# Kernel optimization log

Measured on AMD Instinct MI355X. Metric: run time of the kernel, lower is better.

The kernel has to match this reference:

```python
import jax, jax.numpy as jnp
import numpy as np

EPS = 1e-5
DG = 2  # deformable_groups (num_group)


def conv3x3(x, w):
    return jax.lax.conv_general_dilated(x, w, (1, 1), ((1, 1), (1, 1)),
                                        dimension_numbers=('NCHW', 'OIHW', 'NCHW'))


def bn(x, g, b):
    # training-mode batch norm (batch statistics)
    m = x.mean(axis=(0, 2, 3), keepdims=True)
    v = x.var(axis=(0, 2, 3), keepdims=True)
    return g[None, :, None, None] * (x - m) / jnp.sqrt(v + EPS) + b[None, :, None, None]


def mod_deform_conv(x, w_off, b_off, w, b, dg):
    # ModulatedDeformConvPack: 3x3, stride 1, pad 1
    B, C, H, W = x.shape
    K = 9
    Cg = C // dg
    om = conv3x3(x, w_off) + b_off[None, :, None, None]        # [B, 3*dg*K, H, W]
    o1, o2, m = jnp.split(om, 3, axis=1)
    offy = o1.reshape(B, dg, K, H, W)
    offx = o2.reshape(B, dg, K, H, W)
    mask = jax.nn.sigmoid(m).reshape(B, dg, K, H, W)
    ky = (jnp.arange(K) // 3 - 1).astype(x.dtype)
    kx = (jnp.arange(K) % 3 - 1).astype(x.dtype)
    hh = jnp.arange(H, dtype=x.dtype)
    ww = jnp.arange(W, dtype=x.dtype)
    # fractional sample positions per tap: [B, dg, K, H, W]
    py = hh[None, None, None, :, None] + ky[None, None, :, None, None] + offy
    px = ww[None, None, None, None, :] + kx[None, None, :, None, None] + offx
    y0 = jnp.floor(py)
    x0 = jnp.floor(px)
    ly = py - y0
    lx = px - x0
    y0i = y0.astype(jnp.int32)
    x0i = x0.astype(jnp.int32)
    xg = x.reshape(B, dg, Cg, H * W)

    def gather(yi, xi):
        valid = ((yi >= 0) & (yi < H) & (xi >= 0) & (xi < W)).astype(x.dtype)
        idx = jnp.clip(yi, 0, H - 1) * W + jnp.clip(xi, 0, W - 1)
        flat = idx.reshape(B, dg, 1, K * H * W)
        v = jnp.take_along_axis(xg, flat, axis=3).reshape(B, dg, Cg, K, H, W)
        return v * valid[:, :, None]

    w00 = ((1 - ly) * (1 - lx))[:, :, None]
    w01 = ((1 - ly) * lx)[:, :, None]
    w10 = (ly * (1 - lx))[:, :, None]
    w11 = (ly * lx)[:, :, None]
    val = (gather(y0i, x0i) * w00 + gather(y0i, x0i + 1) * w01 +
           gather(y0i + 1, x0i) * w10 + gather(y0i + 1, x0i + 1) * w11)
    val = val * mask[:, :, None]                               # [B, dg, Cg, K, H, W]
    O = w.shape[0]
    out = jnp.einsum('ogck,bgckhw->bohw', w.reshape(O, dg, Cg, K), val)
    return out + b[None, :, None, None]


def setup_inputs() -> dict:
    key = jax.random.key(0)
    ks = jax.random.split(key, 24)
    B, inC, H, W = 64, 3, 64, 64
    K = 9
    d = {}
    d['x'] = jax.random.normal(ks[0], (B, inC, H, W), dtype=jnp.float32)
    d['conv1_w'] = jax.random.normal(ks[1], (8, inC, 3, 3), jnp.float32) * 0.1
    d['bn1_g'] = jnp.ones((8,), jnp.float32)
    d['bn1_b'] = jnp.zeros((8,), jnp.float32)
    d['conv2_w'] = jax.random.normal(ks[2], (20, 8, 3, 3), jnp.float32) * 0.1
    d['conv2_b'] = jnp.zeros((20,), jnp.float32)
    d['bn2_g'] = jnp.ones((20,), jnp.float32)
    d['bn2_b'] = jnp.zeros((20,), jnp.float32)
    d['off1_w'] = jax.random.normal(ks[3], (3 * DG * K, 20, 3, 3), jnp.float32) * 0.01
    d['off1_b'] = jnp.zeros((3 * DG * K,), jnp.float32)
    d['d1_w'] = jax.random.normal(ks[4], (40, 20, 3, 3), jnp.float32) * 0.05
    d['d1_b'] = jnp.zeros((40,), jnp.float32)
    d['bn3_g'] = jnp.ones((40,), jnp.float32)
    d['bn3_b'] = jnp.zeros((40,), jnp.float32)
    d['off2_w'] = jax.random.normal(ks[5], (3 * DG * K, 40, 3, 3), jnp.float32) * 0.01
    d['off2_b'] = jnp.zeros((3 * DG * K,), jnp.float32)
    d['d2_w'] = jax.random.normal(ks[6], (64, 40, 3, 3), jnp.float32) * 0.05
    d['d2_b'] = jnp.zeros((64,), jnp.float32)
    d['bn4_g'] = jnp.ones((64,), jnp.float32)
    d['bn4_b'] = jnp.zeros((64,), jnp.float32)
    d['fc_w'] = jax.random.normal(ks[7], (10, 256), jnp.float32) * 0.05
    d['fc_b'] = jnp.zeros((10,), jnp.float32)
    return d


def reference(x, conv1_w, bn1_g, bn1_b, conv2_w, conv2_b, bn2_g, bn2_b,
              off1_w, off1_b, d1_w, d1_b, bn3_g, bn3_b,
              off2_w, off2_b, d2_w, d2_b, bn4_g, bn4_b, fc_w, fc_b):
    h = bn(jax.nn.relu(conv3x3(x, conv1_w)), bn1_g, bn1_b)
    h = bn(jax.nn.relu(conv3x3(h, conv2_w) + conv2_b[None, :, None, None]), bn2_g, bn2_b)
    h = bn(jax.nn.relu(mod_deform_conv(h, off1_w, off1_b, d1_w, d1_b, DG)), bn3_g, bn3_b)
    h = bn(jax.nn.relu(mod_deform_conv(h, off2_w, off2_b, d2_w, d2_b, DG)), bn4_g, bn4_b)
    em = h
    B, C, H, W = h.shape
    # avg_pool2d with kernel [H//2, W//2] -> 2x2 spatial output
    p = h.reshape(B, C, 2, H // 2, 2, W // 2).mean(axis=(3, 5)).reshape(B, C * 4)
    logits = p @ fc_w.T + fc_b
    return jax.nn.softmax(logits, axis=1), em
```

## Files before the change

### kernel.cpp

```cpp
#include <hip/hip_runtime.h>
#include <math.h>

#define B_  64
#define H_  64
#define W_  64
#define HW  4096
#define NPIX 262144.0f

__global__ __launch_bounds__(256) void wtr_k(
    const float* __restrict__ w, float* __restrict__ wT, int O, int CK)
{
    const int i = blockIdx.x * 256 + threadIdx.x;
    if (i < O * CK) {
        const int o = i / CK, ck = i - o * CK;
        wT[ck * O + o] = w[i];
    }
}

template<int CT>
__device__ __forceinline__ void stats_accum(
    const float* res, float* sacc, float* ls, int tid)
{
    if (tid < 2 * CT) ls[tid] = 0.f;
    __syncthreads();
#pragma unroll
    for (int o = 0; o < CT; ++o) {
        float s = res[o], s2 = res[o] * res[o];
        for (int off = 32; off; off >>= 1) {
            s  += __shfl_down(s,  off);
            s2 += __shfl_down(s2, off);
        }
        if ((tid & 63) == 0) {
            atomicAdd(&ls[2 * o],     s);
            atomicAdd(&ls[2 * o + 1], s2);
        }
    }
    __syncthreads();
    if (tid < 2 * CT) atomicAdd(&sacc[tid], ls[tid]);
}

template<int C>
__global__ __launch_bounds__(64) void bn_fin_k(
    const float* __restrict__ sacc, float* __restrict__ st)
{
    const int t = threadIdx.x;
    if (t < C) {
        const float mean = sacc[2 * t] / NPIX;
        const float var  = sacc[2 * t + 1] / NPIX - mean * mean;
        st[t]     = mean;
        st[C + t] = rsqrtf(var + 1e-5f);
    }
}

__global__ __launch_bounds__(256) void conv1_k(
    const float* __restrict__ x, const float* __restrict__ w,
    float* __restrict__ out, float* __restrict__ sacc)
{
    const int tid = threadIdx.x;
    const int pix = blockIdx.x * 256 + tid;
    const int b   = blockIdx.y;
    const int h   = pix >> 6, ww = pix & 63;

    float acc[8];
#pragma unroll
    for (int o = 0; o < 8; ++o) acc[o] = 0.f;

#pragma unroll
    for (int ci = 0; ci < 3; ++ci) {
        const float* xp = x + ((size_t)b * 3 + ci) * HW;
#pragma unroll
        for (int t = 0; t < 9; ++t) {
            const int yy = h + t / 3 - 1, xx = ww + t % 3 - 1;
            const bool ok = (yy >= 0) && (yy < 64) && (xx >= 0) && (xx < 64);
            const float xv = ok ? xp[min(max(yy,0),63) * 64 + min(max(xx,0),63)] : 0.f;
#pragma unroll
            for (int o = 0; o < 8; ++o)
                acc[o] = fmaf(w[o * 27 + ci * 9 + t], xv, acc[o]);
        }
    }

    float res[8];
    float* ob = out + (size_t)b * 8 * HW + pix;
#pragma unroll
    for (int o = 0; o < 8; ++o) {
        res[o] = fmaxf(acc[o], 0.f);
        ob[(size_t)o * HW] = res[o];
    }

    __shared__ float ls[16];
    stats_accum<8>(res, sacc, ls, tid);
}

template<int CIN, int COUT, bool RELU, bool STATS>
__global__ __launch_bounds__(256, 4) void convn_k(
    const float* __restrict__ x, const float* __restrict__ wT,
    const float* __restrict__ bias, const float* __restrict__ st,
    const float* __restrict__ gg, const float* __restrict__ bb,
    float* __restrict__ out, float* __restrict__ sacc)
{
    const int tid = threadIdx.x;
    const int pix = blockIdx.x * 256 + tid;
    const int b   = blockIdx.y;
    const int h   = pix >> 6, ww = pix & 63;

    int  tpix[9];
    bool tok[9];
#pragma unroll
    for (int t = 0; t < 9; ++t) {
        const int yy = h + t / 3 - 1, xx = ww + t % 3 - 1;
        tok[t]  = (yy >= 0) && (yy < 64) && (xx >= 0) && (xx < 64);
        tpix[t] = min(max(yy, 0), 63) * 64 + min(max(xx, 0), 63);
    }

    float acc[COUT];
#pragma unroll
    for (int o = 0; o < COUT; ++o) acc[o] = bias[o];

    const float* xb = x + (size_t)b * CIN * HW;

    for (int ci = 0; ci < CIN; ++ci) {
        const float mean = st[ci], rstd = st[CIN + ci];
        const float a  = gg[ci] * rstd;
        const float cc = bb[ci] - gg[ci] * mean * rstd;
        const float* xp = xb + (size_t)ci * HW;

        float xv[9];
#pragma unroll
        for (int t = 0; t < 9; ++t)
            xv[t] = tok[t] ? fmaf(a, xp[tpix[t]], cc) : 0.f;

#pragma unroll
        for (int t = 0; t < 9; ++t) {
            const float* wp = wT + (ci * 9 + t) * COUT;
#pragma unroll
            for (int o = 0; o < COUT; ++o)
                acc[o] = fmaf(wp[o], xv[t], acc[o]);
        }
    }

    float res[COUT];
    float* ob = out + (size_t)b * COUT * HW + pix;
#pragma unroll
    for (int o = 0; o < COUT; ++o) {
        res[o] = RELU ? fmaxf(acc[o], 0.f) : acc[o];
        ob[(size_t)o * HW] = res[o];
    }

    if (STATS) {
        __shared__ float ls[2 * COUT];
        stats_accum<COUT>(res, sacc, ls, tid);
    }
}

template<int CG, int O, int VL, bool STATS>
__global__ __launch_bounds__(256, 4) void deform_k(
    const float* __restrict__ x, const float* __restrict__ om,
    const float* __restrict__ wT, const float* __restrict__ bias,
    const float* __restrict__ st, const float* __restrict__ gg,
    const float* __restrict__ bb,
    float* __restrict__ out, float* __restrict__ sacc)
{
    constexpr int CIN = 2 * CG;
    const int tid = threadIdx.x;
    const int pix = blockIdx.x * 256 + tid;
    const int b   = blockIdx.y;
    const int h   = pix >> 6, ww = pix & 63;

    float acc[O];
#pragma unroll
    for (int o = 0; o < O; ++o) acc[o] = bias[o];

    const float* omb = om + (size_t)b * 54 * HW + pix;
    const float* xb  = x + (size_t)b * CIN * HW;

    for (int g = 0; g < 2; ++g) {
#pragma unroll
        for (int k = 0; k < 9; ++k) {
            const int gk = g * 9 + k;
            const float offy = omb[(size_t)gk * HW];
            const float offx = omb[(size_t)(18 + gk) * HW];
            const float mraw = omb[(size_t)(36 + gk) * HW];
            const float msk  = 1.f / (1.f + __expf(-mraw));

            const float py = (float)(h + k / 3 - 1) + offy;
            const float px = (float)(ww + k % 3 - 1) + offx;
            const float y0f = floorf(py), x0f = floorf(px);
            const float ly = py - y0f, lx = px - x0f;
            const int y0 = (int)y0f, x0 = (int)x0f;
            const int y1 = y0 + 1,  x1 = x0 + 1;

            const bool y0ok = (y0 >= 0) && (y0 < 64);
            const bool y1ok = (y1 >= 0) && (y1 < 64);
            const bool x0ok = (x0 >= 0) && (x0 < 64);
            const bool x1ok = (x1 >= 0) && (x1 < 64);

            float w00 = (1.f-ly)*(1.f-lx)*msk; if (!(y0ok&&x0ok)) w00 = 0.f;
            float w01 = (1.f-ly)*lx      *msk; if (!(y0ok&&x1ok)) w01 = 0.f;
            float w10 = ly*(1.f-lx)      *msk; if (!(y1ok&&x0ok)) w10 = 0.f;
            float w11 = ly*lx            *msk; if (!(y1ok&&x1ok)) w11 = 0.f;
            const float wsum = w00 + w01 + w10 + w11;

            const int i00 = min(max(y0,0),63) * 64 + min(max(x0,0),63);
            const int dx  = (min(max(x1,0),63) - min(max(x0,0),63));
            const int dy  = (min(max(y1,0),63) - min(max(y0,0),63)) * 64;

            for (int cb = 0; cb < CG / VL; ++cb) {
                const int c0 = g * CG + cb * VL;

                float v00[VL], v01[VL], v10[VL], v11[VL];
#pragma unroll
                for (int j = 0; j < VL; ++j) {
                    const float* xp = xb + (size_t)(c0 + j) * HW + i00;
                    v00[j] = xp[0];
                    v01[j] = xp[dx];
                    v10[j] = xp[dy];
                    v11[j] = xp[dy + dx];
                }

                float val[VL];
#pragma unroll
                for (int j = 0; j < VL; ++j) {
                    const float mean = st[c0 + j], rstd = st[CIN + c0 + j];
                    const float a  = gg[c0 + j] * rstd;
                    const float cc = bb[c0 + j] - gg[c0 + j] * mean * rstd;
                    const float gath = w00*v00[j] + w01*v01[j] +
                                       w10*v10[j] + w11*v11[j];
                    val[j] = fmaf(a, gath, cc * wsum);
                }

                const float* wp0 = wT + ((c0 + 0) * 9 + k) * O;
                const float* wp1 = wT + ((c0 + 1) * 9 + k) * O;
#pragma unroll
                for (int o = 0; o < O; ++o) {
                    float t = acc[o];
                    t = fmaf(wp0[o], val[0], t);
                    t = fmaf(wp1[o], val[1], t);
                    if (VL == 4) {
                        t = fmaf(wp1[O * 9 + o], val[2], t);
                        t = fmaf(wp1[2 * O * 9 + o], val[3], t);
                    }
                    acc[o] = t;
                }
            }
        }
    }

    float res[O];
    float* ob = out + (size_t)b * O * HW + pix;
#pragma unroll
    for (int o = 0; o < O; ++o) {
        res[o] = fmaxf(acc[o], 0.f);
        ob[(size_t)o * HW] = res[o];
    }

    if (STATS) {
        __shared__ float ls[2 * O];
        stats_accum<O>(res, sacc, ls, tid);
    }
}

__global__ __launch_bounds__(256) void bn_apply4_k(
    float* __restrict__ y, const float* __restrict__ st,
    const float* __restrict__ gg, const float* __restrict__ bb)
{
    const size_t i4 = (size_t)blockIdx.x * 256 + threadIdx.x;
    const int c = (int)((i4 >> 10) & 63);
    const float m = st[c], r = st[64 + c];
    const float a = gg[c] * r, cc = bb[c] - gg[c] * m * r;
    float4 v = ((float4*)y)[i4];
    v.x = a*v.x + cc; v.y = a*v.y + cc; v.z = a*v.z + cc; v.w = a*v.w + cc;
    ((float4*)y)[i4] = v;
}

__global__ __launch_bounds__(256) void pool_k(
    const float* __restrict__ em, float* __restrict__ pooled)
{
    const int b = blockIdx.x, c = blockIdx.y, t = threadIdx.x;
    const int q = t >> 6, l = t & 63;
    const float* p = em + ((size_t)b * 64 + c) * HW + (q >> 1) * 32 * W_ + (q & 1) * 32;
    float s = 0.f;
    for (int i = l; i < 1024; i += 64) {
        const int yy = i >> 5, xx = i & 31;
        s += p[yy * W_ + xx];
    }
    for (int off = 32; off; off >>= 1) s += __shfl_down(s, off);
    if (l == 0) pooled[b * 256 + c * 4 + q] = s * (1.f / 1024.f);
}

__global__ __launch_bounds__(64) void fc_k(
    const float* __restrict__ pooled, const float* __restrict__ fcw,
    const float* __restrict__ fcb, float* __restrict__ out)
{
    const int b = blockIdx.x, t = threadIdx.x;
    __shared__ float logits[10];
    if (t < 10) {
        float l = fcb[t];
        const float* p = pooled + b * 256;
        for (int j = 0; j < 256; ++j) l += fcw[t * 256 + j] * p[j];
        logits[t] = l;
    }
    __syncthreads();
    if (t == 0) {
        float mx = logits[0];
        for (int i = 1; i < 10; ++i) mx = fmaxf(mx, logits[i]);
        float e[10]; float sum = 0.f;
        for (int i = 0; i < 10; ++i) { e[i] = __expf(logits[i] - mx); sum += e[i]; }
        const float inv = 1.f / sum;
        for (int i = 0; i < 10; ++i) out[b * 10 + i] = e[i] * inv;
    }
}

extern "C" void kernel_launch(void* const* d_in, const int* in_sizes, int n_in,
                              void* d_out, int out_size, void* d_ws, size_t ws_size,
                              hipStream_t stream)
{
    const float* x       = (const float*)d_in[0];
    const float* conv1_w = (const float*)d_in[1];
    const float* bn1_g   = (const float*)d_in[2];
    const float* bn1_b   = (const float*)d_in[3];
    const float* conv2_w = (const float*)d_in[4];
    const float* conv2_b = (const float*)d_in[5];
    const float* bn2_g   = (const float*)d_in[6];
    const float* bn2_b   = (const float*)d_in[7];
    const float* off1_w  = (const float*)d_in[8];
    const float* off1_b  = (const float*)d_in[9];
    const float* d1_w    = (const float*)d_in[10];
    const float* d1_b    = (const float*)d_in[11];
    const float* bn3_g   = (const float*)d_in[12];
    const float* bn3_b   = (const float*)d_in[13];
    const float* off2_w  = (const float*)d_in[14];
    const float* off2_b  = (const float*)d_in[15];
    const float* d2_w    = (const float*)d_in[16];
    const float* d2_b    = (const float*)d_in[17];
    const float* bn4_g   = (const float*)d_in[18];
    const float* bn4_b   = (const float*)d_in[19];
    const float* fc_w    = (const float*)d_in[20];
    const float* fc_b    = (const float*)d_in[21];

    float* ws = (float*)d_ws;
    float* Bb = ws;
    float* D  = ws + 5242880;
    float* C  = ws + 15728640;
    float* A  = C;
    float* sm = ws + 29884416;
    float* s1 = sm,        *s2 = sm + 16,  *s3 = sm + 56,  *s4 = sm + 136;
    float* st1 = sm + 264, *st2 = sm + 280, *st3 = sm + 320, *st4 = sm + 400;
    float* pooled = sm + 528;
    float* c2T = sm + 16912;
    float* o1T = sm + 18352;
    float* o2T = sm + 28072;
    float* d1T = sm + 47512;
    float* d2T = sm + 54712;

    float* outp = (float*)d_out;
    float* em   = outp + 640;

    const dim3 blk(256);
    const dim3 gpix(16, B_);

    hipMemsetAsync(sm, 0, 264 * sizeof(float), stream);

    wtr_k<<<(20*72  + 255)/256, blk, 0, stream>>>(conv2_w, c2T, 20, 72);
    wtr_k<<<(54*180 + 255)/256, blk, 0, stream>>>(off1_w,  o1T, 54, 180);
    wtr_k<<<(54*360 + 255)/256, blk, 0, stream>>>(off2_w,  o2T, 54, 360);
    wtr_k<<<(40*180 + 255)/256, blk, 0, stream>>>(d1_w,    d1T, 40, 180);
    wtr_k<<<(64*360 + 255)/256, blk, 0, stream>>>(d2_w,    d2T, 64, 360);

    conv1_k<<<gpix, blk, 0, stream>>>(x, conv1_w, A, s1);
    bn_fin_k<8><<<1, 64, 0, stream>>>(s1, st1);

    convn_k<8, 20, true, true><<<gpix, blk, 0, stream>>>(
        A, c2T, conv2_b, st1, bn1_g, bn1_b, Bb, s2);
    bn_fin_k<20><<<1, 64, 0, stream>>>(s2, st2);

    convn_k<20, 54, false, false><<<gpix, blk, 0, stream>>>(
        Bb, o1T, off1_b, st2, bn2_g, bn2_b, C, nullptr);
    deform_k<10, 40, 2, true><<<gpix, blk, 0, stream>>>(
        Bb, C, d1T, d1_b, st2, bn2_g, bn2_b, D, s3);
    bn_fin_k<40><<<1, 64, 0, stream>>>(s3, st3);

    convn_k<40, 54, false, false><<<gpix, blk, 0, stream>>>(
        D, o2T, off2_b, st3, bn3_g, bn3_b, C, nullptr);
    deform_k<20, 64, 4, true><<<gpix, blk, 0, stream>>>(
        D, C, d2T, d2_b, st3, bn3_g, bn3_b, em, s4);
    bn_fin_k<64><<<1, 64, 0, stream>>>(s4, st4);

    bn_apply4_k<<<16384, blk, 0, stream>>>(em, st4, bn4_g, bn4_b);

    pool_k<<<dim3(B_, 64), blk, 0, stream>>>(em, pooled);
    fc_k<<<B_, 64, 0, stream>>>(pooled, fc_w, fc_b, outp);
}
```

Before: 889.8 us.

## Use packed fp16 dot2 with channel-paired weights in conv and deform kernels

Weights are repacked into fp16 pairs of adjacent input channels, and activations are converted to packed half2 so each FMA pair becomes one v_dot2 instruction accumulating in fp32. BN scale/shift per channel is precomputed into shared memory once per block instead of being recomputed inside the loops, and the convn loop order is swapped to tap-outer. This halves the inner-loop ALU instruction count and weight load bandwidth, but reduces input and weight precision to fp16, which could raise numerical error. Full unrolling also increases code size and register pressure.

```diff
diff --git a/kernel.cpp b/kernel.cpp
--- a/kernel.cpp
+++ b/kernel.cpp
@@ -7,13 +7,23 @@
 #define HW  4096
 #define NPIX 262144.0f
 
-__global__ __launch_bounds__(256) void wtr_k(
-    const float* __restrict__ w, float* __restrict__ wT, int O, int CK)
+typedef __fp16 h2 __attribute__((ext_vector_type(2)));
+
+__global__ __launch_bounds__(256) void wpack_k(
+    const float* __restrict__ w, h2* __restrict__ wp, int O, int C)
 {
     const int i = blockIdx.x * 256 + threadIdx.x;
-    if (i < O * CK) {
-        const int o = i / CK, ck = i - o * CK;
-        wT[ck * O + o] = w[i];
+    const int total = 9 * (C / 2) * O;
+    if (i < total) {
+        const int o    = i % O;
+        const int rest = i / O;
+        const int cp   = rest % (C / 2);
+        const int t    = rest / (C / 2);
+        const int c    = 2 * cp;
+        h2 p;
+        p.x = (__fp16)w[o * (C * 9) + c * 9 + t];
+        p.y = (__fp16)w[o * (C * 9) + (c + 1) * 9 + t];
+        wp[i] = p;
     }
 }
 
@@ -93,7 +103,7 @@
 
 template<int CIN, int COUT, bool RELU, bool STATS>
 __global__ __launch_bounds__(256, 4) void convn_k(
-    const float* __restrict__ x, const float* __restrict__ wT,
+    const float* __restrict__ x, const h2* __restrict__ wp,
     const float* __restrict__ bias, const float* __restrict__ st,
     const float* __restrict__ gg, const float* __restrict__ bb,
     float* __restrict__ out, float* __restrict__ sacc)
@@ -103,6 +113,14 @@
     const int b   = blockIdx.y;
     const int h   = pix >> 6, ww = pix & 63;
 
+    __shared__ float lsa[CIN], lsc[CIN];
+    if (tid < CIN) {
+        const float mean = st[tid], rstd = st[CIN + tid];
+        lsa[tid] = gg[tid] * rstd;
+        lsc[tid] = bb[tid] - gg[tid] * mean * rstd;
+    }
+    __syncthreads();
+
     int  tpix[9];
     bool tok[9];
 #pragma unroll
@@ -118,23 +136,22 @@
 
     const float* xb = x + (size_t)b * CIN * HW;
 
-    for (int ci = 0; ci < CIN; ++ci) {
-        const float mean = st[ci], rstd = st[CIN + ci];
-        const float a  = gg[ci] * rstd;
-        const float cc = bb[ci] - gg[ci] * mean * rstd;
-        const float* xp = xb + (size_t)ci * HW;
-
-        float xv[9];
-#pragma unroll
-        for (int t = 0; t < 9; ++t)
-            xv[t] = tok[t] ? fmaf(a, xp[tpix[t]], cc) : 0.f;
-
-#pragma unroll
-        for (int t = 0; t < 9; ++t) {
-            const float* wp = wT + (ci * 9 + t) * COUT;
+#pragma unroll
+    for (int t = 0; t < 9; ++t) {
+        const float* xq = xb + tpix[t];
+        const bool ok = tok[t];
+#pragma unroll
+        for (int cp = 0; cp < CIN / 2; ++cp) {
+            const int c = 2 * cp;
+            const float x0 = xq[(size_t)c * HW];
+            const float x1 = xq[(size_t)(c + 1) * HW];
+            const float v0 = ok ? fmaf(lsa[c],     x0, lsc[c])     : 0.f;
+            const float v1 = ok ? fmaf(lsa[c + 1], x1, lsc[c + 1]) : 0.f;
+            const h2 val2 = __builtin_amdgcn_cvt_pkrtz(v0, v1);
+            const h2* wrow = wp + (t * (CIN / 2) + cp) * COUT;
 #pragma unroll
             for (int o = 0; o < COUT; ++o)
-                acc[o] = fmaf(wp[o], xv[t], acc[o]);
+                acc[o] = __builtin_amdgcn_fdot2(val2, wrow[o], acc[o], false);
         }
     }
 
@@ -152,10 +169,10 @@
     }
 }
 
-template<int CG, int O, int VL, bool STATS>
+template<int CG, int O, bool STATS>
 __global__ __launch_bounds__(256, 4) void deform_k(
     const float* __restrict__ x, const float* __restrict__ om,
-    const float* __restrict__ wT, const float* __restrict__ bias,
+    const h2* __restrict__ wp, const float* __restrict__ bias,
     const float* __restrict__ st, const float* __restrict__ gg,
     const float* __restrict__ bb,
     float* __restrict__ out, float* __restrict__ sacc)
@@ -165,6 +182,14 @@
     const int pix = blockIdx.x * 256 + tid;
     const int b   = blockIdx.y;
     const int h   = pix >> 6, ww = pix & 63;
+
+    __shared__ float lsa[CIN], lsc[CIN];
+    if (tid < CIN) {
+        const float mean = st[tid], rstd = st[CIN + tid];
+        lsa[tid] = gg[tid] * rstd;
+        lsc[tid] = bb[tid] - gg[tid] * mean * rstd;
+    }
+    __syncthreads();
 
     float acc[O];
 #pragma unroll
@@ -204,43 +229,27 @@
             const int dx  = (min(max(x1,0),63) - min(max(x0,0),63));
             const int dy  = (min(max(y1,0),63) - min(max(y0,0),63)) * 64;
 
-            for (int cb = 0; cb < CG / VL; ++cb) {
-                const int c0 = g * CG + cb * VL;
-
-                float v00[VL], v01[VL], v10[VL], v11[VL];
-#pragma unroll
-                for (int j = 0; j < VL; ++j) {
-                    const float* xp = xb + (size_t)(c0 + j) * HW + i00;
-                    v00[j] = xp[0];
-                    v01[j] = xp[dx];
-                    v10[j] = xp[dy];
-                    v11[j] = xp[dy + dx];
-                }
-
-                float val[VL];
-#pragma unroll
-                for (int j = 0; j < VL; ++j) {
-                    const float mean = st[c0 + j], rstd = st[CIN + c0 + j];
-                    const float a  = gg[c0 + j] * rstd;
-                    const float cc = bb[c0 + j] - gg[c0 + j] * mean * rstd;
-                    const float gath = w00*v00[j] + w01*v01[j] +
-                                       w10*v10[j] + w11*v11[j];
-                    val[j] = fmaf(a, gath, cc * wsum);
-                }
-
-                const float* wp0 = wT + ((c0 + 0) * 9 + k) * O;
-                const float* wp1 = wT + ((c0 + 1) * 9 + k) * O;
-#pragma unroll
-                for (int o = 0; o < O; ++o) {
-                    float t = acc[o];
-                    t = fmaf(wp0[o], val[0], t);
-                    t = fmaf(wp1[o], val[1], t);
-                    if (VL == 4) {
-                        t = fmaf(wp1[O * 9 + o], val[2], t);
-                        t = fmaf(wp1[2 * O * 9 + o], val[3], t);
-                    }
-                    acc[o] = t;
-                }
+#pragma unroll
+            for (int cp = 0; cp < CG / 2; ++cp) {
+                const int c = g * CG + 2 * cp;
+                const float* xp0 = xb + (size_t)c * HW + i00;
+                const float* xp1 = xp0 + HW;
+
+                const float a00 = xp0[0],  a01 = xp0[dx];
+                const float a10 = xp0[dy], a11 = xp0[dy + dx];
+                const float b00 = xp1[0],  b01 = xp1[dx];
+                const float b10 = xp1[dy], b11 = xp1[dy + dx];
+
+                const float g0 = w00*a00 + w01*a01 + w10*a10 + w11*a11;
+                const float g1 = w00*b00 + w01*b01 + w10*b10 + w11*b11;
+                const float v0 = fmaf(lsa[c],     g0, lsc[c]     * wsum);
+                const float v1 = fmaf(lsa[c + 1], g1, lsc[c + 1] * wsum);
+                const h2 val2 = __builtin_amdgcn_cvt_pkrtz(v0, v1);
+
+                const h2* wrow = wp + (k * (CIN / 2) + (c >> 1)) * O;
+#pragma unroll
+                for (int o = 0; o < O; ++o)
+                    acc[o] = __builtin_amdgcn_fdot2(val2, wrow[o], acc[o], false);
             }
         }
     }
@@ -346,11 +355,11 @@
     float* s1 = sm,        *s2 = sm + 16,  *s3 = sm + 56,  *s4 = sm + 136;
     float* st1 = sm + 264, *st2 = sm + 280, *st3 = sm + 320, *st4 = sm + 400;
     float* pooled = sm + 528;
-    float* c2T = sm + 16912;
-    float* o1T = sm + 18352;
-    float* o2T = sm + 28072;
-    float* d1T = sm + 47512;
-    float* d2T = sm + 54712;
+    h2* c2P = (h2*)(sm + 16912);
+    h2* o1P = (h2*)(sm + 17632);
+    h2* o2P = (h2*)(sm + 22492);
+    h2* d1P = (h2*)(sm + 32212);
+    h2* d2P = (h2*)(sm + 35812);
 
     float* outp = (float*)d_out;
     float* em   = outp + 640;
@@ -358,31 +367,31 @@
     const dim3 blk(256);
     const dim3 gpix(16, B_);
 
-    hipMemsetAsync(sm, 0, 264 * sizeof(float), stream);
-
-    wtr_k<<<(20*72  + 255)/256, blk, 0, stream>>>(conv2_w, c2T, 20, 72);
-    wtr_k<<<(54*180 + 255)/256, blk, 0, stream>>>(off1_w,  o1T, 54, 180);
-    wtr_k<<<(54*360 + 255)/256, blk, 0, stream>>>(off2_w,  o2T, 54, 360);
-    wtr_k<<<(40*180 + 255)/256, blk, 0, stream>>>(d1_w,    d1T, 40, 180);
-    wtr_k<<<(64*360 + 255)/256, blk, 0, stream>>>(d2_w,    d2T, 64, 360);
+    (void)hipMemsetAsync(sm, 0, 264 * sizeof(float), stream);
+
+    wpack_k<<<(720   + 255)/256, blk, 0, stream>>>(conv2_w, c2P, 20, 8);
+    wpack_k<<<(4860  + 255)/256, blk, 0, stream>>>(off1_w,  o1P, 54, 20);
+    wpack_k<<<(9720  + 255)/256, blk, 0, stream>>>(off2_w,  o2P, 54, 40);
+    wpack_k<<<(3600  + 255)/256, blk, 0, stream>>>(d1_w,    d1P, 40, 20);
+    wpack_k<<<(11520 + 255)/256, blk, 0, stream>>>(d2_w,    d2P, 64, 40);
 
     conv1_k<<<gpix, blk, 0, stream>>>(x, conv1_w, A, s1);
     bn_fin_k<8><<<1, 64, 0, stream>>>(s1, st1);
 
     convn_k<8, 20, true, true><<<gpix, blk, 0, stream>>>(
-        A, c2T, conv2_b, st1, bn1_g, bn1_b, Bb, s2);
+        A, c2P, conv2_b, st1, bn1_g, bn1_b, Bb, s2);
     bn_fin_k<20><<<1, 64, 0, stream>>>(s2, st2);
 
     convn_k<20, 54, false, false><<<gpix, blk, 0, stream>>>(
-        Bb, o1T, off1_b, st2, bn2_g, bn2_b, C, nullptr);
-    deform_k<10, 40, 2, true><<<gpix, blk, 0, stream>>>(
-        Bb, C, d1T, d1_b, st2, bn2_g, bn2_b, D, s3);
+        Bb, o1P, off1_b, st2, bn2_g, bn2_b, C, nullptr);
+    deform_k<10, 40, true><<<gpix, blk, 0, stream>>>(
+        Bb, C, d1P, d1_b, st2, bn2_g, bn2_b, D, s3);
     bn_fin_k<40><<<1, 64, 0, stream>>>(s3, st3);
 
     convn_k<40, 54, false, false><<<gpix, blk, 0, stream>>>(
-        D, o2T, off2_b, st3, bn3_g, bn3_b, C, nullptr);
-    deform_k<20, 64, 4, true><<<gpix, blk, 0, stream>>>(
-        D, C, d2T, d2_b, st3, bn3_g, bn3_b, em, s4);
+        D, o2P, off2_b, st3, bn3_g, bn3_b, C, nullptr);
+    deform_k<20, 64, true><<<gpix, blk, 0, stream>>>(
+        D, C, d2P, d2_b, st3, bn3_g, bn3_b, em, s4);
     bn_fin_k<64><<<1, 64, 0, stream>>>(s4, st4);
 
     bn_apply4_k<<<16384, blk, 0, stream>>>(em, st4, bn4_g, bn4_b);
```

After: 2.482 ms. +178.9%, slower.
